# Kernel optimization log

Measured on AMD Instinct MI355X. Metric: run time of the kernel, lower is better.

Reference implementation:

```python
import jax, jax.numpy as jnp
import numpy as np

K = 2  # number of SGConv propagation hops


def setup_inputs() -> dict:
    key = jax.random.key(0)
    k1, k2, k3, k4 = jax.random.split(key, 4)
    N, E, T, H = 50000, 800000, 256, 128
    x = jax.random.normal(k1, (N, T), dtype=jnp.float32)
    edge_index = jax.random.randint(k2, (2, E), 0, N, dtype=jnp.int64)
    edge_weights = jax.random.normal(k3, (E,), dtype=jnp.float32)
    W = jax.random.normal(k4, (H, T), dtype=jnp.float32) * 0.05
    b = jnp.zeros((H,), dtype=jnp.float32)
    return {"x": x, "edge_index": edge_index, "edge_weights": edge_weights, "W": W, "b": b}


def reference(x, edge_index, edge_weights, W, b):
    N = x.shape[0]
    # in-place clamp from forward(): weights with elu(w) <= 0 are set to 1e-7
    ew = jnp.where(jax.nn.elu(edge_weights) <= 0, jnp.float32(1e-7), edge_weights)

    # gcn_norm with add_self_loops=True (fill_value = 1.0)
    loop = jnp.arange(N, dtype=edge_index.dtype)
    row = jnp.concatenate([edge_index[0], loop])  # source nodes
    col = jnp.concatenate([edge_index[1], loop])  # target nodes (aggregation index)
    w = jnp.concatenate([ew, jnp.ones((N,), dtype=ew.dtype)])

    deg = jax.ops.segment_sum(w, col, num_segments=N)          # [N]
    dis = jnp.where(deg > 0, jax.lax.rsqrt(deg), jnp.float32(0.0))
    norm = dis[row] * w * dis[col]                             # [E+N]

    # K-hop propagation: h <- scatter_add(norm * h[src]) at dst
    h = x
    for _ in range(K):
        h = jax.ops.segment_sum(h[row] * norm[:, None], col, num_segments=N)

    # final linear transform of SGConv
    return h @ W.T + b
```

## Files before the change

kernel.cpp:

```cpp
#include <hip/hip_runtime.h>


typedef __attribute__((ext_vector_type(8))) short short8_t;
typedef __attribute__((ext_vector_type(4))) float f32x4_t;

constexpr int BK    = 256;
constexpr int CAP   = 8192;
constexpr int CHUNK = 4096;

__device__ inline unsigned short f2bf(float f) {
    unsigned int u = __float_as_uint(f);
    return (unsigned short)((u + 0x7fffu + ((u >> 16) & 1u)) >> 16);
}
__device__ inline float bf_lo(unsigned int u) { return __uint_as_float(u << 16); }
__device__ inline float bf_hi(unsigned int u) { return __uint_as_float(u & 0xffff0000u); }

__global__ __launch_bounds__(256) void k_passA(
    const int* __restrict__ rows, const int* __restrict__ cols,
    const float* __restrict__ ew, int E,
    unsigned int* __restrict__ bwr,
    unsigned char* __restrict__ bcl,
    int* __restrict__ tails,
    const float* __restrict__ W, unsigned short* __restrict__ Wbf, int WT)
{
    const int tid = threadIdx.x;
    const int gid = blockIdx.x * 256 + tid;
    if (gid < WT) Wbf[gid] = f2bf(W[gid]);

    __shared__ unsigned short lcol[CHUNK], lrow[CHUNK], lw[CHUNK];
    __shared__ unsigned short sidx[CHUNK];
    __shared__ int hist[256], lofs[256], fill[256], gbase[256];

    const int e0  = blockIdx.x * CHUNK;
    const int cnt = min(CHUNK, E - e0);
    if (cnt <= 0) return;

    hist[tid] = 0; fill[tid] = 0;
    __syncthreads();

    for (int i = tid; i < cnt; i += 256) {
        const int c = cols[e0 + i];
        const int r = rows[e0 + i];
        float w = ew[e0 + i];
        w = (w > 0.0f) ? w : 1e-7f;
        lcol[i] = (unsigned short)c;
        lrow[i] = (unsigned short)r;
        lw[i]   = f2bf(w);
        atomicAdd(&hist[c >> 8], 1);
    }
    __syncthreads();

    {
        const int v = hist[tid];
        lofs[tid] = v;
        __syncthreads();
        for (int off = 1; off < 256; off <<= 1) {
            int t = (tid >= off) ? lofs[tid - off] : 0;
            __syncthreads();
            lofs[tid] += t;
            __syncthreads();
        }
        const int excl = lofs[tid] - v;
        __syncthreads();
        lofs[tid] = excl;
        __syncthreads();
    }

    for (int i = tid; i < cnt; i += 256) {
        const int b = lcol[i] >> 8;
        const int pos = lofs[b] + atomicAdd(&fill[b], 1);
        sidx[pos] = (unsigned short)i;
    }
    __syncthreads();

    {
        const int h = hist[tid];
        gbase[tid] = (h > 0) ? atomicAdd(&tails[tid], h) : 0;
    }
    __syncthreads();

    for (int i = tid; i < cnt; i += 256) {
        const int e = sidx[i];
        const int b = lcol[e] >> 8;
        const int slot = gbase[b] + (i - lofs[b]);
        if (slot < CAP) {
            const int addr = b * CAP + slot;
            bwr[addr] = ((unsigned int)lw[e] << 16) | lrow[e];
            bcl[addr] = (unsigned char)(lcol[e] & 255);
        }
    }
}

__global__ __launch_bounds__(256) void k_passB(
    const unsigned int* __restrict__ bwr, const unsigned char* __restrict__ bcl,
    const int* __restrict__ tails,
    unsigned int* __restrict__ meta, int* __restrict__ starts,
    int* __restrict__ ends, float* __restrict__ dis, int N)
{
    const int tid  = threadIdx.x;
    const int b    = blockIdx.x;
    const int base = b * CAP;
    const int cnt  = min(tails[b], CAP);

    __shared__ unsigned int  lwr[CAP];
    __shared__ unsigned char lcl[CAP];
    __shared__ unsigned int  srt[CAP];
    __shared__ int hist[256], offs[256], fill[256];

    hist[tid] = 0; fill[tid] = 0;
    __syncthreads();

    for (int i = tid; i < cnt; i += 256) {
        lwr[i] = bwr[base + i];
        unsigned char c = bcl[base + i];
        lcl[i] = c;
        atomicAdd(&hist[c], 1);
    }
    __syncthreads();

    {
        const int v = hist[tid];
        offs[tid] = v;
        __syncthreads();
        for (int off = 1; off < 256; off <<= 1) {
            int t = (tid >= off) ? offs[tid - off] : 0;
            __syncthreads();
            offs[tid] += t;
            __syncthreads();
        }
        const int excl = offs[tid] - v;
        __syncthreads();
        offs[tid] = excl;
        __syncthreads();
    }

    for (int i = tid; i < cnt; i += 256) {
        const int c = lcl[i];
        const int pos = offs[c] + atomicAdd(&fill[c], 1);
        srt[pos] = lwr[i];
    }
    __syncthreads();

    for (int i = tid; i < cnt; i += 256) meta[base + i] = srt[i];

    const int node = b * BK + tid;
    if (node < N) {
        const int s = offs[tid];
        const int t = s + hist[tid];
        float sum = 1.0f;
        for (int j = s; j < t; ++j) sum += bf_hi(srt[j]);
        dis[node]    = rsqrtf(sum);
        starts[node] = base + s;
        ends[node]   = base + t;
    }
}

__global__ __launch_bounds__(256) void k_transform_mfma(
    const float* __restrict__ x, const unsigned short* __restrict__ Wbf,
    const float* __restrict__ dis, unsigned short* __restrict__ z, int N)
{
    constexpr int RB  = 64;
    constexpr int LDK = 264;
    __shared__ unsigned short xs[RB][LDK];

    const int tid = threadIdx.x;
    const int r0  = blockIdx.x * RB;

    {
        const float4* x4 = reinterpret_cast<const float4*>(x);
        for (int i = tid; i < RB * 64; i += 256) {
            const int rr  = i >> 6;
            const int c4  = i & 63;
            const int row = r0 + rr;
            float4 v = make_float4(0.f, 0.f, 0.f, 0.f);
            if (row < N) v = x4[(size_t)row * 64 + c4];
            unsigned short* p = &xs[rr][c4 * 4];
            p[0] = f2bf(v.x); p[1] = f2bf(v.y);
            p[2] = f2bf(v.z); p[3] = f2bf(v.w);
        }
    }
    __syncthreads();

    const int wave = tid >> 6;
    const int lane = tid & 63;
    const int lr   = lane & 15;
    const int kg   = lane >> 4;
    const int wr0  = wave * 16;

    f32x4_t acc[8];
#pragma unroll
    for (int n = 0; n < 8; ++n) acc[n] = (f32x4_t){0.f, 0.f, 0.f, 0.f};

    for (int k0 = 0; k0 < 256; k0 += 32) {
        const int kb = k0 + kg * 8;
        short8_t af = *reinterpret_cast<const short8_t*>(&xs[wr0 + lr][kb]);
#pragma unroll
        for (int n = 0; n < 8; ++n) {
            short8_t bf = *reinterpret_cast<const short8_t*>(
                Wbf + (size_t)(n * 16 + lr) * 256 + kb);
            acc[n] = __builtin_amdgcn_mfma_f32_16x16x32_bf16(af, bf, acc[n], 0, 0, 0);
        }
    }

    float dsc[4];
#pragma unroll
    for (int r = 0; r < 4; ++r) {
        const int orow = r0 + wr0 + kg * 4 + r;
        dsc[r] = (orow < N) ? dis[orow] : 0.f;
    }
#pragma unroll
    for (int n = 0; n < 8; ++n) {
#pragma unroll
        for (int r = 0; r < 4; ++r) {
            const int orow = r0 + wr0 + kg * 4 + r;
            if (orow < N)
                z[(size_t)orow * 128 + n * 16 + lr] = f2bf(dsc[r] * acc[n][r]);
        }
    }
}

template <bool FINAL>
__global__ __launch_bounds__(256) void k_hop(
    const int* __restrict__ starts, const int* __restrict__ ends,
    const unsigned int* __restrict__ meta,
    const float* __restrict__ dis, const unsigned int* __restrict__ hin,
    const float* __restrict__ bias, void* __restrict__ hout, int N)
{
    const int wave = threadIdx.x >> 6;
    const int lane = threadIdx.x & 63;
    const int node = blockIdx.x * 4 + wave;
    if (node >= N) return;

    const int s = __builtin_amdgcn_readfirstlane(starts[node]);
    const int t = __builtin_amdgcn_readfirstlane(ends[node]);
    const float d = dis[node];

    unsigned int v = hin[(size_t)node * 64 + lane];
    float ax = bf_lo(v), ay = bf_hi(v);

    int j = s;
    for (; j + 8 <= t; j += 8) {
        unsigned int m0 = meta[j],     m1 = meta[j + 1];
        unsigned int m2 = meta[j + 2], m3 = meta[j + 3];
        unsigned int m4 = meta[j + 4], m5 = meta[j + 5];
        unsigned int m6 = meta[j + 6], m7 = meta[j + 7];
        unsigned int u0 = hin[(size_t)(m0 & 0xffffu) * 64 + lane];
        unsigned int u1 = hin[(size_t)(m1 & 0xffffu) * 64 + lane];
        unsigned int u2 = hin[(size_t)(m2 & 0xffffu) * 64 + lane];
        unsigned int u3 = hin[(size_t)(m3 & 0xffffu) * 64 + lane];
        unsigned int u4 = hin[(size_t)(m4 & 0xffffu) * 64 + lane];
        unsigned int u5 = hin[(size_t)(m5 & 0xffffu) * 64 + lane];
        unsigned int u6 = hin[(size_t)(m6 & 0xffffu) * 64 + lane];
        unsigned int u7 = hin[(size_t)(m7 & 0xffffu) * 64 + lane];
        ax += bf_hi(m0) * bf_lo(u0); ay += bf_hi(m0) * bf_hi(u0);
        ax += bf_hi(m1) * bf_lo(u1); ay += bf_hi(m1) * bf_hi(u1);
        ax += bf_hi(m2) * bf_lo(u2); ay += bf_hi(m2) * bf_hi(u2);
        ax += bf_hi(m3) * bf_lo(u3); ay += bf_hi(m3) * bf_hi(u3);
        ax += bf_hi(m4) * bf_lo(u4); ay += bf_hi(m4) * bf_hi(u4);
        ax += bf_hi(m5) * bf_lo(u5); ay += bf_hi(m5) * bf_hi(u5);
        ax += bf_hi(m6) * bf_lo(u6); ay += bf_hi(m6) * bf_hi(u6);
        ax += bf_hi(m7) * bf_lo(u7); ay += bf_hi(m7) * bf_hi(u7);
    }
    for (; j < t; ++j) {
        unsigned int m = meta[j];
        const float w = bf_hi(m);
        unsigned int u = hin[(size_t)(m & 0xffffu) * 64 + lane];
        ax += w * bf_lo(u); ay += w * bf_hi(u);
    }

    if (FINAL) {
        float2 bv = reinterpret_cast<const float2*>(bias)[lane];
        float2 o; o.x = d * ax + bv.x; o.y = d * ay + bv.y;
        reinterpret_cast<float2*>(hout)[(size_t)node * 64 + lane] = o;
    } else {
        const float d2 = d * d;
        unsigned int p = (unsigned int)f2bf(d2 * ax) |
                         ((unsigned int)f2bf(d2 * ay) << 16);
        reinterpret_cast<unsigned int*>(hout)[(size_t)node * 64 + lane] = p;
    }
}

extern "C" void kernel_launch(void* const* d_in, const int* in_sizes, int n_in,
                              void* d_out, int out_size, void* d_ws, size_t ws_size,
                              hipStream_t stream)
{
    const float* x  = (const float*)d_in[0];
    const int*   ei = (const int*)d_in[1];
    const float* ew = (const float*)d_in[2];
    const float* W  = (const float*)d_in[3];
    const float* b  = (const float*)d_in[4];

    const int E  = in_sizes[2];
    const int H  = in_sizes[4];
    const int T  = in_sizes[3] / H;
    const int N  = in_sizes[0] / T;
    const int WT = in_sizes[3];
    const int NB = (N + BK - 1) / BK;

    const int* rows = ei;
    const int* cols = ei + E;

    char* wsb = (char*)d_ws;
    unsigned int*   z    = (unsigned int*)wsb;   wsb += (size_t)N * (H / 2) * 4;
    unsigned int*   z1   = (unsigned int*)wsb;   wsb += (size_t)N * (H / 2) * 4;
    unsigned int*   meta = (unsigned int*)wsb;   wsb += (size_t)NB * CAP * 4;
    unsigned short* Wbf  = (unsigned short*)wsb; wsb += (size_t)WT * 2;
    float*          dis  = (float*)wsb;          wsb += (size_t)N * 4;
    int*            sta  = (int*)wsb;            wsb += (size_t)N * 4;
    int*            end_ = (int*)wsb;            wsb += (size_t)N * 4;
    int*            tails= (int*)wsb;            wsb += (size_t)NB * 4;
    unsigned int*   bwr  = z1;
    unsigned char*  bcl  = (unsigned char*)(z1 + (size_t)NB * CAP);

    float* out = (float*)d_out;

    hipMemsetAsync(tails, 0, (size_t)NB * 4, stream);
    {
        const int nblkA = (E + CHUNK - 1) / CHUNK;
        k_passA<<<nblkA, 256, 0, stream>>>(rows, cols, ew, E,
                                           bwr, bcl, tails, W, Wbf, WT);
        k_passB<<<NB, 256, 0, stream>>>(bwr, bcl, tails,
                                        meta, sta, end_, dis, N);
    }

    {
        const int RB = 64;
        k_transform_mfma<<<(N + RB - 1) / RB, 256, 0, stream>>>(
            x, Wbf, dis, (unsigned short*)z, N);
    }

    const int gH = (N + 3) / 4;
    k_hop<false><<<gH, 256, 0, stream>>>(sta, end_, meta, dis, z, nullptr, z1, N);
    k_hop<true ><<<gH, 256, 0, stream>>>(sta, end_, meta, dis, z1, b, out, N);
}
```

Measured before the change: 141.9 us.

## Split transform GEMM across waves by output columns and preload W into registers

The MFMA transform kernel now uses 32-row tiles with four waves arranged as 2 row groups by 2 column halves. Each wave preloads its slice of bf16 W into registers before staging x, so the inner loop reads W from registers instead of issuing global loads. Launch bounds ask for 2 blocks per SM and the grid doubles. In exchange, register pressure rises (32 short8 fragments per lane), and W is re-read from global or cache by twice as many blocks.

```diff
diff --git a/kernel.cpp b/kernel.cpp
--- a/kernel.cpp
+++ b/kernel.cpp
@@ -155,16 +155,30 @@
     }
 }
 
-__global__ __launch_bounds__(256) void k_transform_mfma(
+__global__ __launch_bounds__(256, 2) void k_transform_mfma(
     const float* __restrict__ x, const unsigned short* __restrict__ Wbf,
     const float* __restrict__ dis, unsigned short* __restrict__ z, int N)
 {
-    constexpr int RB  = 64;
+    constexpr int RB  = 32;
     constexpr int LDK = 264;
     __shared__ unsigned short xs[RB][LDK];
 
-    const int tid = threadIdx.x;
-    const int r0  = blockIdx.x * RB;
+    const int tid  = threadIdx.x;
+    const int r0   = blockIdx.x * RB;
+    const int wave = tid >> 6;
+    const int lane = tid & 63;
+    const int lr   = lane & 15;
+    const int kg   = lane >> 4;
+    const int nb   = (wave & 1) * 4;
+    const int wr0  = (wave >> 1) * 16;
+
+    short8_t wf[4][8];
+#pragma unroll
+    for (int n = 0; n < 4; ++n)
+#pragma unroll
+        for (int k = 0; k < 8; ++k)
+            wf[n][k] = *reinterpret_cast<const short8_t*>(
+                Wbf + (size_t)((nb + n) * 16 + lr) * 256 + k * 32 + kg * 8);
 
     {
         const float4* x4 = reinterpret_cast<const float4*>(x);
@@ -181,25 +195,18 @@
     }
     __syncthreads();
 
-    const int wave = tid >> 6;
-    const int lane = tid & 63;
-    const int lr   = lane & 15;
-    const int kg   = lane >> 4;
-    const int wr0  = wave * 16;
-
-    f32x4_t acc[8];
-#pragma unroll
-    for (int n = 0; n < 8; ++n) acc[n] = (f32x4_t){0.f, 0.f, 0.f, 0.f};
-
-    for (int k0 = 0; k0 < 256; k0 += 32) {
-        const int kb = k0 + kg * 8;
-        short8_t af = *reinterpret_cast<const short8_t*>(&xs[wr0 + lr][kb]);
-#pragma unroll
-        for (int n = 0; n < 8; ++n) {
-            short8_t bf = *reinterpret_cast<const short8_t*>(
-                Wbf + (size_t)(n * 16 + lr) * 256 + kb);
-            acc[n] = __builtin_amdgcn_mfma_f32_16x16x32_bf16(af, bf, acc[n], 0, 0, 0);
-        }
+    f32x4_t acc[4];
+#pragma unroll
+    for (int n = 0; n < 4; ++n) acc[n] = (f32x4_t){0.f, 0.f, 0.f, 0.f};
+
+#pragma unroll
+    for (int k = 0; k < 8; ++k) {
+        const short8_t af =
+            *reinterpret_cast<const short8_t*>(&xs[wr0 + lr][k * 32 + kg * 8]);
+#pragma unroll
+        for (int n = 0; n < 4; ++n)
+            acc[n] = __builtin_amdgcn_mfma_f32_16x16x32_bf16(af, wf[n][k],
+                                                             acc[n], 0, 0, 0);
     }
 
     float dsc[4];
@@ -209,12 +216,13 @@
         dsc[r] = (orow < N) ? dis[orow] : 0.f;
     }
 #pragma unroll
-    for (int n = 0; n < 8; ++n) {
+    for (int n = 0; n < 4; ++n) {
 #pragma unroll
         for (int r = 0; r < 4; ++r) {
             const int orow = r0 + wr0 + kg * 4 + r;
             if (orow < N)
-                z[(size_t)orow * 128 + n * 16 + lr] = f2bf(dsc[r] * acc[n][r]);
+                z[(size_t)orow * 128 + (nb + n) * 16 + lr] =
+                    f2bf(dsc[r] * acc[n][r]);
         }
     }
 }
@@ -324,7 +332,7 @@
     }
 
     {
-        const int RB = 64;
+        const int RB = 32;
         k_transform_mfma<<<(N + RB - 1) / RB, 256, 0, stream>>>(
             x, Wbf, dis, (unsigned short*)z, N);
     }
```

Measured after the change: 139.8 us. About the same (-1.5%).
